# Kernel optimization log

Hardware: AMD Instinct MI355X
Metric: run time of the kernel (lower is better)

## Reference

```python
import jax, jax.numpy as jnp
import numpy as np

NUM_GRAPHS = 1024


def _mlp2(h, Wa, ba, Wb, bb):
    # Linear -> ReLU -> Linear
    return jax.nn.relu(h @ Wa + ba) @ Wb + bb


def setup_inputs() -> dict:
    key = jax.random.key(0)
    ks = jax.random.split(key, 16)
    N, F, H, C, E = 100000, 128, 128, 10, 1600000
    x = jax.random.normal(ks[0], (N, F), dtype=jnp.float32)
    edge_index = jax.random.randint(ks[1], (2, E), 0, N, dtype=jnp.int64)
    batch = jnp.sort(jax.random.randint(ks[2], (N,), 0, NUM_GRAPHS, dtype=jnp.int64))
    s = 1.0 / np.sqrt(H)
    def w(k, shape):
        return jax.random.uniform(k, shape, jnp.float32, -s, s)
    return {
        "x": x, "edge_index": edge_index, "batch": batch,
        "W1a": w(ks[3], (F, H)), "b1a": w(ks[4], (H,)),
        "W1b": w(ks[5], (H, H)), "b1b": w(ks[6], (H,)),
        "W2a": w(ks[7], (H, H)), "b2a": w(ks[8], (H,)),
        "W2b": w(ks[9], (H, H)), "b2b": w(ks[10], (H,)),
        "Wl1": w(ks[11], (H, H)), "bl1": w(ks[12], (H,)),
        "Wl2": w(ks[13], (H, C)), "bl2": w(ks[14], (C,)),
    }


def reference(x, edge_index, batch, W1a, b1a, W1b, b1b, W2a, b2a, W2b, b2b, Wl1, bl1, Wl2, bl2):
    N = x.shape[0]
    src, dst = edge_index[0], edge_index[1]

    def gin_conv(h, Wa, ba, Wb, bb):
        # sum-aggregate neighbor features: agg[i] = sum_{(src->dst=i)} h[src]
        agg = jax.ops.segment_sum(h[src], dst, num_segments=N)
        # eps = 0 (PyG default): nn((1+eps)*h + agg)
        return _mlp2(h + agg, Wa, ba, Wb, bb)

    h = jax.nn.relu(gin_conv(x, W1a, b1a, W1b, b1b))
    h = jax.nn.relu(gin_conv(h, W2a, b2a, W2b, b2b))
    # global_add_pool over graph ids -> [num_graphs, H]
    g = jax.ops.segment_sum(h, batch, num_segments=NUM_GRAPHS)
    g = jax.nn.relu(g @ Wl1 + bl1)
    return jax.nn.log_softmax(g @ Wl2 + bl2, axis=1)
```

## Files before the change

### kernel.cpp

```cpp
#include <hip/hip_runtime.h>
#include <hip/hip_bf16.h>
#include <math.h>

#define NUM_GRAPHS 1024

typedef __attribute__((ext_vector_type(8))) short bf16x8;
typedef __attribute__((ext_vector_type(4))) float f32x4;

static __device__ __forceinline__ unsigned short f2bf(float f) {
    union { float f; unsigned u; } v; v.f = f;
    unsigned r = v.u + 0x7fffu + ((v.u >> 16) & 1u);
    return (unsigned short)(r >> 16);
}
static __device__ __forceinline__ float bf_lo(unsigned u) { return __uint_as_float(u << 16); }
static __device__ __forceinline__ float bf_hi(unsigned u) { return __uint_as_float(u & 0xffff0000u); }

__global__ void k_pre(const int* __restrict__ eiDst, int E,
                      int* __restrict__ deg, int* __restrict__ rank,
                      const float* __restrict__ x, int n4, unsigned* __restrict__ xb,
                      int eb) {
    if ((int)blockIdx.x < eb) {
        int e = blockIdx.x * 256 + threadIdx.x;
        if (e < E) rank[e] = atomicAdd(&deg[eiDst[e]], 1);
    } else {
        int i = (blockIdx.x - eb) * 256 + threadIdx.x;
        int stride = (gridDim.x - eb) * 256;
        const float4* x4 = (const float4*)x;
        for (; i < n4; i += stride) {
            float4 v = x4[i];
            unsigned lo = (unsigned)f2bf(v.x) | ((unsigned)f2bf(v.y) << 16);
            unsigned hi = (unsigned)f2bf(v.z) | ((unsigned)f2bf(v.w) << 16);
            ((uint2*)xb)[i] = make_uint2(lo, hi);
        }
    }
}

__global__ void k_scan1(const int* __restrict__ deg, int N,
                        int* __restrict__ excl, int* __restrict__ bsum) {
    __shared__ int s[256];
    int i = blockIdx.x * 256 + threadIdx.x;
    int v = (i < N) ? deg[i] : 0;
    s[threadIdx.x] = v;
    __syncthreads();
    for (int off = 1; off < 256; off <<= 1) {
        int t = (threadIdx.x >= off) ? s[threadIdx.x - off] : 0;
        __syncthreads();
        s[threadIdx.x] += t;
        __syncthreads();
    }
    if (i < N) excl[i] = s[threadIdx.x] - v;
    if (threadIdx.x == 255) bsum[blockIdx.x] = s[255];
}

__global__ void k_scan2(int* __restrict__ bsum, int nb) {
    __shared__ int s[1024];
    int t = threadIdx.x;
    int v = (t < nb) ? bsum[t] : 0;
    s[t] = v;
    __syncthreads();
    for (int off = 1; off < 1024; off <<= 1) {
        int u = (t >= off) ? s[t - off] : 0;
        __syncthreads();
        s[t] += u;
        __syncthreads();
    }
    if (t < nb) bsum[t] = s[t] - v;
}

__global__ void k_scan3(const int* __restrict__ excl, const int* __restrict__ bsum,
                        int N, int E, int* __restrict__ rp) {
    int i = blockIdx.x * 256 + threadIdx.x;
    if (i < N) rp[i] = excl[i] + bsum[i >> 8];
    if (i == 0) rp[N] = E;
}

#define FILL_PASSES 3
#define FILL_RANGE 33334
__global__ void k_fill3(const int* __restrict__ ei, const int* __restrict__ rank,
                        int E, const int* __restrict__ rp, int* __restrict__ srcs) {
    const int tid0 = blockIdx.x * 256 + threadIdx.x;
    const int stride = gridDim.x * 256;
    for (int pass = 0; pass < FILL_PASSES; ++pass) {
        const int lo = pass * FILL_RANGE;
        const int hi = lo + FILL_RANGE;
        for (int e = tid0; e < E; e += stride) {
            int d = ei[(size_t)E + e];
            if (d >= lo && d < hi) {
                srcs[rp[d] + rank[e]] = ei[e];
            }
        }
    }
}

__global__ void k_prepw4(const float* __restrict__ W0, const float* __restrict__ W1,
                         const float* __restrict__ W2, const float* __restrict__ W3,
                         unsigned short* __restrict__ wt) {
    int b = blockIdx.x >> 6;
    const float* W = (b == 0) ? W0 : (b == 1) ? W1 : (b == 2) ? W2 : W3;
    int idx = (blockIdx.x & 63) * 256 + threadIdx.x;
    int k = idx >> 7, n = idx & 127;
    wt[b * 16384 + n * 128 + k] = f2bf(W[idx]);
}

__device__ __forceinline__ void acc8(float* a, uint4 v) {
    a[0] += bf_lo(v.x); a[1] += bf_hi(v.x);
    a[2] += bf_lo(v.y); a[3] += bf_hi(v.y);
    a[4] += bf_lo(v.z); a[5] += bf_hi(v.z);
    a[6] += bf_lo(v.w); a[7] += bf_hi(v.w);
}

__global__ __launch_bounds__(256, 8)
void k_aggq(const uint4* __restrict__ H4, const int* __restrict__ rp,
            const int* __restrict__ srcs, int N, uint4* __restrict__ out) {
    int gw = (blockIdx.x * blockDim.x + threadIdx.x) >> 6;
    int lane = threadIdx.x & 63;
    int q = lane >> 4, ql = lane & 15;
    int n = gw * 4 + q;
    if (gw * 4 >= N) return;
    bool act = (n < N);
    int nc = act ? n : 0;
    uint4 s0 = H4[(size_t)nc * 16 + ql];
    float a[8];
    a[0] = bf_lo(s0.x); a[1] = bf_hi(s0.x);
    a[2] = bf_lo(s0.y); a[3] = bf_hi(s0.y);
    a[4] = bf_lo(s0.z); a[5] = bf_hi(s0.z);
    a[6] = bf_lo(s0.w); a[7] = bf_hi(s0.w);
    int j = act ? rp[nc] : 0;
    int e = act ? rp[nc + 1] : 0;
    while (j + 4 <= e) {
        int i0 = srcs[j], i1 = srcs[j + 1], i2 = srcs[j + 2], i3 = srcs[j + 3];
        uint4 v0 = H4[(size_t)i0 * 16 + ql];
        uint4 v1 = H4[(size_t)i1 * 16 + ql];
        uint4 v2 = H4[(size_t)i2 * 16 + ql];
        uint4 v3 = H4[(size_t)i3 * 16 + ql];
        acc8(a, v0); acc8(a, v1); acc8(a, v2); acc8(a, v3);
        j += 4;
    }
    while (j < e) {
        uint4 v = H4[(size_t)srcs[j] * 16 + ql];
        acc8(a, v);
        ++j;
    }
    if (act) {
        uint4 o;
        o.x = (unsigned)f2bf(a[0]) | ((unsigned)f2bf(a[1]) << 16);
        o.y = (unsigned)f2bf(a[2]) | ((unsigned)f2bf(a[3]) << 16);
        o.z = (unsigned)f2bf(a[4]) | ((unsigned)f2bf(a[5]) << 16);
        o.w = (unsigned)f2bf(a[6]) | ((unsigned)f2bf(a[7]) << 16);
        out[(size_t)n * 16 + ql] = o;
    }
}

__device__ __forceinline__ int swz_base(int row, int chunk) {
    return row * 128 + ((chunk ^ (row & 7)) << 3);
}

__global__ __launch_bounds__(256, 2)
void k_mlp(const unsigned short* __restrict__ U, int N,
           const unsigned short* __restrict__ WaT, const float* __restrict__ ba,
           const unsigned short* __restrict__ WbT, const float* __restrict__ bb,
           unsigned short* __restrict__ Y) {
    __shared__ unsigned short lA[128 * 128];
    __shared__ unsigned short lW[128 * 128];

    const int tid = threadIdx.x;
    const int lane = tid & 63;
    const int w = tid >> 6;
    const int wr = (w >> 1) * 64;
    const int wc = (w & 1) * 64;
    const int r0 = blockIdx.x * 128;

    {
        const uint4* U4 = (const uint4*)U;
        #pragma unroll
        for (int i = 0; i < 8; ++i) {
            int c = tid + 256 * i;
            int row = c >> 4, q = c & 15;
            uint4 v = (r0 + row < N) ? U4[(size_t)(r0 + row) * 16 + q]
                                     : make_uint4(0u, 0u, 0u, 0u);
            *(uint4*)&lA[swz_base(row, q)] = v;
        }
    }
    {
        const uint4* Wsrc = (const uint4*)WaT;
        #pragma unroll
        for (int i = 0; i < 8; ++i) {
            int c = tid + 256 * i;
            int row = c >> 4, q = c & 15;
            *(uint4*)&lW[swz_base(row, q)] = Wsrc[c];
        }
    }
    __syncthreads();

    const int am = lane & 15;
    const int kq = (lane >> 4) * 8;

    f32x4 acc[4][4];
    #pragma unroll
    for (int i = 0; i < 4; ++i)
        #pragma unroll
        for (int j = 0; j < 4; ++j) acc[i][j] = (f32x4){0.f, 0.f, 0.f, 0.f};

    #pragma unroll
    for (int ks = 0; ks < 4; ++ks) {
        int k0 = ks * 32 + kq;
        bf16x8 af[4], bq[4];
        #pragma unroll
        for (int i = 0; i < 4; ++i)
            af[i] = *(const bf16x8*)&lA[swz_base(wr + i * 16 + am, k0 >> 3)];
        #pragma unroll
        for (int j = 0; j < 4; ++j)
            bq[j] = *(const bf16x8*)&lW[swz_base(wc + j * 16 + am, k0 >> 3)];
        #pragma unroll
        for (int i = 0; i < 4; ++i)
            #pragma unroll
            for (int j = 0; j < 4; ++j)
                acc[i][j] = __builtin_amdgcn_mfma_f32_16x16x32_bf16(af[i], bq[j], acc[i][j], 0, 0, 0);
    }
    __syncthreads();

    #pragma unroll
    for (int j = 0; j < 4; ++j) {
        int col = wc + j * 16 + am;
        float bias = ba[col];
        #pragma unroll
        for (int i = 0; i < 4; ++i) {
            int rowb = wr + i * 16 + (lane >> 4) * 4;
            #pragma unroll
            for (int r = 0; r < 4; ++r) {
                float t = acc[i][j][r] + bias;
                t = t > 0.f ? t : 0.f;
                int row = rowb + r;
                lA[swz_base(row, col >> 3) + (col & 7)] = f2bf(t);
            }
        }
    }
    {
        const uint4* Wsrc = (const uint4*)WbT;
        #pragma unroll
        for (int i = 0; i < 8; ++i) {
            int c = tid + 256 * i;
            int row = c >> 4, q = c & 15;
            *(uint4*)&lW[swz_base(row, q)] = Wsrc[c];
        }
    }
    __syncthreads();

    #pragma unroll
    for (int i = 0; i < 4; ++i)
        #pragma unroll
        for (int j = 0; j < 4; ++j) acc[i][j] = (f32x4){0.f, 0.f, 0.f, 0.f};

    #pragma unroll
    for (int ks = 0; ks < 4; ++ks) {
        int k0 = ks * 32 + kq;
        bf16x8 af[4], bq[4];
        #pragma unroll
        for (int i = 0; i < 4; ++i)
            af[i] = *(const bf16x8*)&lA[swz_base(wr + i * 16 + am, k0 >> 3)];
        #pragma unroll
        for (int j = 0; j < 4; ++j)
            bq[j] = *(const bf16x8*)&lW[swz_base(wc + j * 16 + am, k0 >> 3)];
        #pragma unroll
        for (int i = 0; i < 4; ++i)
            #pragma unroll
            for (int j = 0; j < 4; ++j)
                acc[i][j] = __builtin_amdgcn_mfma_f32_16x16x32_bf16(af[i], bq[j], acc[i][j], 0, 0, 0);
    }

    #pragma unroll
    for (int j = 0; j < 4; ++j) {
        int col = wc + j * 16 + am;
        float bias = bb[col];
        #pragma unroll
        for (int i = 0; i < 4; ++i) {
            int rowb = wr + i * 16 + (lane >> 4) * 4;
            #pragma unroll
            for (int r = 0; r < 4; ++r) {
                int row = r0 + rowb + r;
                if (row < N) {
                    float t = acc[i][j][r] + bias;
                    t = t > 0.f ? t : 0.f;
                    Y[(size_t)row * 128 + col] = f2bf(t);
                }
            }
        }
    }
}

#define PSTRIP 8
__global__ void k_pool(const unsigned* __restrict__ H, const int* __restrict__ batch,
                       int N, float* __restrict__ G) {
    int wid = (blockIdx.x * blockDim.x + threadIdx.x) >> 6;
    int lane = threadIdx.x & 63;
    int n0 = wid * PSTRIP;
    if (n0 >= N) return;
    int n1 = n0 + PSTRIP; if (n1 > N) n1 = N;
    const size_t fo = (size_t)lane * 2;
    int cur = batch[n0];
    float aL = 0.f, aH = 0.f;
    for (int n = n0; n < n1; ++n) {
        int b = batch[n];
        if (b != cur) {
            atomicAdd(&G[(size_t)cur * 128 + fo], aL);
            atomicAdd(&G[(size_t)cur * 128 + fo + 1], aH);
            aL = 0.f; aH = 0.f;
            cur = b;
        }
        unsigned v = H[(size_t)n * 64 + lane];
        aL += bf_lo(v);
        aH += bf_hi(v);
    }
    atomicAdd(&G[(size_t)cur * 128 + fo], aL);
    atomicAdd(&G[(size_t)cur * 128 + fo + 1], aH);
}

__global__ void k_head(const float* __restrict__ G,
                       const float* __restrict__ Wl1, const float* __restrict__ bl1,
                       const float* __restrict__ Wl2, const float* __restrict__ bl2,
                       int C, float* __restrict__ out) {
    __shared__ float sg[128];
    __shared__ float sh[128];
    __shared__ float sl[16];
    int row = blockIdx.x;
    int t = threadIdx.x;
    sg[t] = G[(size_t)row * 128 + t];
    __syncthreads();
    float a = bl1[t];
    for (int k = 0; k < 128; ++k) a += sg[k] * Wl1[k * 128 + t];
    sh[t] = a > 0.f ? a : 0.f;
    __syncthreads();
    if (t < C) {
        float l = bl2[t];
        for (int k = 0; k < 128; ++k) l += sh[k] * Wl2[k * C + t];
        sl[t] = l;
    }
    __syncthreads();
    if (t < C) {
        float m = -1e30f;
        for (int j = 0; j < C; ++j) m = fmaxf(m, sl[j]);
        float s = 0.f;
        for (int j = 0; j < C; ++j) s += __expf(sl[j] - m);
        out[(size_t)row * C + t] = sl[t] - m - __logf(s);
    }
}

extern "C" void kernel_launch(void* const* d_in, const int* in_sizes, int n_in,
                              void* d_out, int out_size, void* d_ws, size_t ws_size,
                              hipStream_t stream) {
    const float* x    = (const float*)d_in[0];
    const int*   ei   = (const int*)d_in[1];
    const int*   batch= (const int*)d_in[2];
    const float* W1a  = (const float*)d_in[3];
    const float* b1a  = (const float*)d_in[4];
    const float* W1b  = (const float*)d_in[5];
    const float* b1b  = (const float*)d_in[6];
    const float* W2a  = (const float*)d_in[7];
    const float* b2a  = (const float*)d_in[8];
    const float* W2b  = (const float*)d_in[9];
    const float* b2b  = (const float*)d_in[10];
    const float* Wl1  = (const float*)d_in[11];
    const float* bl1  = (const float*)d_in[12];
    const float* Wl2  = (const float*)d_in[13];
    const float* bl2  = (const float*)d_in[14];
    float* out = (float*)d_out;

    const int N = in_sizes[2];
    const int E = in_sizes[1] / 2;
    const int C = in_sizes[13] / 128;

    char* p = (char*)d_ws;
    auto alloc = [&](size_t bytes) {
        char* r = p;
        p += (bytes + 255) & ~(size_t)255;
        return r;
    };
    unsigned* xb = (unsigned*)alloc((size_t)N * 64 * 4);
    unsigned* hA = (unsigned*)alloc((size_t)N * 64 * 4);
    unsigned* hB = (unsigned*)alloc((size_t)N * 64 * 4);
    float* g   = (float*)alloc((size_t)NUM_GRAPHS * 128 * 4);
    int* deg   = (int*)alloc((size_t)N * 4);
    int* excl  = (int*)alloc((size_t)N * 4);
    int* rp    = (int*)alloc((size_t)(N + 1) * 4);
    int* rank  = (int*)alloc((size_t)E * 4);
    int* bsum  = (int*)alloc(4096);
    int* srcs  = (int*)alloc((size_t)E * 4);
    unsigned short* wt = (unsigned short*)alloc((size_t)4 * 16384 * 2);
    (void)ws_size; (void)n_in; (void)out_size;

    const int nb = (N + 255) / 256;
    const int eb = (E + 255) / 256;

    hipMemsetAsync(deg, 0, (size_t)N * 4, stream);
    hipMemsetAsync(g, 0, (size_t)NUM_GRAPHS * 128 * 4, stream);

    k_pre<<<eb + 4096, 256, 0, stream>>>(ei + E, E, deg, rank, x, N * 32, xb, eb);
    k_scan1<<<nb, 256, 0, stream>>>(deg, N, excl, bsum);
    k_scan2<<<1, 1024, 0, stream>>>(bsum, nb);
    k_scan3<<<nb, 256, 0, stream>>>(excl, bsum, N, E, rp);
    k_fill3<<<2048, 256, 0, stream>>>(ei, rank, E, rp, srcs);
    k_prepw4<<<256, 256, 0, stream>>>(W1a, W1b, W2a, W2b, wt);

    const int mb = (N + 127) / 128;
    const int qw = (N + 3) / 4;
    const int qb = (qw + 3) / 4;

    k_aggq<<<qb, 256, 0, stream>>>((const uint4*)xb, rp, srcs, N, (uint4*)hA);
    k_mlp<<<mb, 256, 0, stream>>>((const unsigned short*)hA, N, wt, b1a, wt + 16384, b1b,
                                  (unsigned short*)hB);
    k_aggq<<<qb, 256, 0, stream>>>((const uint4*)hB, rp, srcs, N, (uint4*)hA);
    k_mlp<<<mb, 256, 0, stream>>>((const unsigned short*)hA, N, wt + 2 * 16384, b2a,
                                  wt + 3 * 16384, b2b, (unsigned short*)hB);

    const int pw = (N + PSTRIP - 1) / PSTRIP;
    const int pb = (pw + 3) / 4;
    k_pool<<<pb, 256, 0, stream>>>(hB, batch, N, g);
    k_head<<<NUM_GRAPHS, 128, 0, stream>>>(g, Wl1, bl1, Wl2, bl2, C, out);
}
```

Baseline: 439.1 us.

## Fuse global pooling into second MLP and merge small setup kernels

```diff
diff --git a/kernel.cpp b/kernel.cpp
--- a/kernel.cpp
+++ b/kernel.cpp
@@ -18,13 +18,13 @@
 __global__ void k_pre(const int* __restrict__ eiDst, int E,
                       int* __restrict__ deg, int* __restrict__ rank,
                       const float* __restrict__ x, int n4, unsigned* __restrict__ xb,
-                      int eb) {
+                      float* __restrict__ G, int eb) {
     if ((int)blockIdx.x < eb) {
         int e = blockIdx.x * 256 + threadIdx.x;
         if (e < E) rank[e] = atomicAdd(&deg[eiDst[e]], 1);
-    } else {
+    } else if ((int)blockIdx.x < eb + 4096) {
         int i = (blockIdx.x - eb) * 256 + threadIdx.x;
-        int stride = (gridDim.x - eb) * 256;
+        int stride = 4096 * 256;
         const float4* x4 = (const float4*)x;
         for (; i < n4; i += stride) {
             float4 v = x4[i];
@@ -32,6 +32,11 @@
             unsigned hi = (unsigned)f2bf(v.z) | ((unsigned)f2bf(v.w) << 16);
             ((uint2*)xb)[i] = make_uint2(lo, hi);
         }
+    } else {
+        int i = (blockIdx.x - eb - 4096) * 256 + threadIdx.x;
+        float4* G4 = (float4*)G;
+        for (; i < NUM_GRAPHS * 32; i += 64 * 256)
+            G4[i] = make_float4(0.f, 0.f, 0.f, 0.f);
     }
 }
 
@@ -52,54 +57,58 @@
     if (threadIdx.x == 255) bsum[blockIdx.x] = s[255];
 }
 
-__global__ void k_scan2(int* __restrict__ bsum, int nb) {
-    __shared__ int s[1024];
-    int t = threadIdx.x;
-    int v = (t < nb) ? bsum[t] : 0;
-    s[t] = v;
-    __syncthreads();
-    for (int off = 1; off < 1024; off <<= 1) {
-        int u = (t >= off) ? s[t - off] : 0;
-        __syncthreads();
-        s[t] += u;
-        __syncthreads();
-    }
-    if (t < nb) bsum[t] = s[t] - v;
-}
-
-__global__ void k_scan3(const int* __restrict__ excl, const int* __restrict__ bsum,
-                        int N, int E, int* __restrict__ rp) {
-    int i = blockIdx.x * 256 + threadIdx.x;
-    if (i < N) rp[i] = excl[i] + bsum[i >> 8];
+__global__ void k_scan23(const int* __restrict__ excl, const int* __restrict__ bsum,
+                         int nb, int N, int E, int* __restrict__ rp) {
+    __shared__ int s[512];
+    const int t = threadIdx.x;
+    for (int k = t; k < 512; k += 256) s[k] = (k < nb) ? bsum[k] : 0;
+    __syncthreads();
+    #pragma unroll
+    for (int off = 1; off < 512; off <<= 1) {
+        int a = (t >= off) ? s[t - off] : 0;
+        int b = s[t + 256 - off];
+        __syncthreads();
+        s[t] += a;
+        s[t + 256] += b;
+        __syncthreads();
+    }
+    const int myIncl = s[blockIdx.x];
+    const int myOwn = bsum[blockIdx.x];
+    const int off_b = myIncl - myOwn;
+    int i = blockIdx.x * 256 + t;
+    if (i < N) rp[i] = excl[i] + off_b;
     if (i == 0) rp[N] = E;
 }
 
 #define FILL_PASSES 3
 #define FILL_RANGE 33334
-__global__ void k_fill3(const int* __restrict__ ei, const int* __restrict__ rank,
-                        int E, const int* __restrict__ rp, int* __restrict__ srcs) {
-    const int tid0 = blockIdx.x * 256 + threadIdx.x;
-    const int stride = gridDim.x * 256;
-    for (int pass = 0; pass < FILL_PASSES; ++pass) {
-        const int lo = pass * FILL_RANGE;
-        const int hi = lo + FILL_RANGE;
-        for (int e = tid0; e < E; e += stride) {
-            int d = ei[(size_t)E + e];
-            if (d >= lo && d < hi) {
-                srcs[rp[d] + rank[e]] = ei[e];
+#define FILL_BLOCKS 2048
+__global__ void k_fillprep(const int* __restrict__ ei, const int* __restrict__ rank,
+                           int E, const int* __restrict__ rp, int* __restrict__ srcs,
+                           const float* __restrict__ W0, const float* __restrict__ W1,
+                           const float* __restrict__ W2, const float* __restrict__ W3,
+                           unsigned short* __restrict__ wt) {
+    if ((int)blockIdx.x < FILL_BLOCKS) {
+        const int tid0 = blockIdx.x * 256 + threadIdx.x;
+        const int stride = FILL_BLOCKS * 256;
+        for (int pass = 0; pass < FILL_PASSES; ++pass) {
+            const int lo = pass * FILL_RANGE;
+            const int hi = lo + FILL_RANGE;
+            for (int e = tid0; e < E; e += stride) {
+                int d = ei[(size_t)E + e];
+                if (d >= lo && d < hi) {
+                    srcs[rp[d] + rank[e]] = ei[e];
+                }
             }
         }
-    }
-}
-
-__global__ void k_prepw4(const float* __restrict__ W0, const float* __restrict__ W1,
-                         const float* __restrict__ W2, const float* __restrict__ W3,
-                         unsigned short* __restrict__ wt) {
-    int b = blockIdx.x >> 6;
-    const float* W = (b == 0) ? W0 : (b == 1) ? W1 : (b == 2) ? W2 : W3;
-    int idx = (blockIdx.x & 63) * 256 + threadIdx.x;
-    int k = idx >> 7, n = idx & 127;
-    wt[b * 16384 + n * 128 + k] = f2bf(W[idx]);
+    } else {
+        int lb = blockIdx.x - FILL_BLOCKS;
+        int b = lb >> 6;
+        const float* W = (b == 0) ? W0 : (b == 1) ? W1 : (b == 2) ? W2 : W3;
+        int idx = (lb & 63) * 256 + threadIdx.x;
+        int k = idx >> 7, n = idx & 127;
+        wt[b * 16384 + n * 128 + k] = f2bf(W[idx]);
+    }
 }
 
 __device__ __forceinline__ void acc8(float* a, uint4 v) {
@@ -155,13 +164,16 @@
     return row * 128 + ((chunk ^ (row & 7)) << 3);
 }
 
+template <bool POOL>
 __global__ __launch_bounds__(256, 2)
 void k_mlp(const unsigned short* __restrict__ U, int N,
            const unsigned short* __restrict__ WaT, const float* __restrict__ ba,
            const unsigned short* __restrict__ WbT, const float* __restrict__ bb,
-           unsigned short* __restrict__ Y) {
+           unsigned short* __restrict__ Y,
+           const int* __restrict__ batch, float* __restrict__ G) {
     __shared__ unsigned short lA[128 * 128];
     __shared__ unsigned short lW[128 * 128];
+    __shared__ int bs[128];
 
     const int tid = threadIdx.x;
     const int lane = tid & 63;
@@ -268,51 +280,62 @@
                 acc[i][j] = __builtin_amdgcn_mfma_f32_16x16x32_bf16(af[i], bq[j], acc[i][j], 0, 0, 0);
     }
 
-    #pragma unroll
-    for (int j = 0; j < 4; ++j) {
-        int col = wc + j * 16 + am;
-        float bias = bb[col];
-        #pragma unroll
-        for (int i = 0; i < 4; ++i) {
-            int rowb = wr + i * 16 + (lane >> 4) * 4;
+    if (!POOL) {
+        #pragma unroll
+        for (int j = 0; j < 4; ++j) {
+            int col = wc + j * 16 + am;
+            float bias = bb[col];
             #pragma unroll
-            for (int r = 0; r < 4; ++r) {
-                int row = r0 + rowb + r;
-                if (row < N) {
+            for (int i = 0; i < 4; ++i) {
+                int rowb = wr + i * 16 + (lane >> 4) * 4;
+                #pragma unroll
+                for (int r = 0; r < 4; ++r) {
+                    int row = r0 + rowb + r;
+                    if (row < N) {
+                        float t = acc[i][j][r] + bias;
+                        t = t > 0.f ? t : 0.f;
+                        Y[(size_t)row * 128 + col] = f2bf(t);
+                    }
+                }
+            }
+        }
+    } else {
+        __syncthreads();
+        #pragma unroll
+        for (int j = 0; j < 4; ++j) {
+            int col = wc + j * 16 + am;
+            float bias = bb[col];
+            #pragma unroll
+            for (int i = 0; i < 4; ++i) {
+                int rowb = wr + i * 16 + (lane >> 4) * 4;
+                #pragma unroll
+                for (int r = 0; r < 4; ++r) {
                     float t = acc[i][j][r] + bias;
                     t = t > 0.f ? t : 0.f;
-                    Y[(size_t)row * 128 + col] = f2bf(t);
+                    int row = rowb + r;
+                    lA[swz_base(row, col >> 3) + (col & 7)] = f2bf(t);
                 }
             }
         }
-    }
-}
-
-#define PSTRIP 8
-__global__ void k_pool(const unsigned* __restrict__ H, const int* __restrict__ batch,
-                       int N, float* __restrict__ G) {
-    int wid = (blockIdx.x * blockDim.x + threadIdx.x) >> 6;
-    int lane = threadIdx.x & 63;
-    int n0 = wid * PSTRIP;
-    if (n0 >= N) return;
-    int n1 = n0 + PSTRIP; if (n1 > N) n1 = N;
-    const size_t fo = (size_t)lane * 2;
-    int cur = batch[n0];
-    float aL = 0.f, aH = 0.f;
-    for (int n = n0; n < n1; ++n) {
-        int b = batch[n];
-        if (b != cur) {
-            atomicAdd(&G[(size_t)cur * 128 + fo], aL);
-            atomicAdd(&G[(size_t)cur * 128 + fo + 1], aH);
-            aL = 0.f; aH = 0.f;
-            cur = b;
-        }
-        unsigned v = H[(size_t)n * 64 + lane];
-        aL += bf_lo(v);
-        aH += bf_hi(v);
-    }
-    atomicAdd(&G[(size_t)cur * 128 + fo], aL);
-    atomicAdd(&G[(size_t)cur * 128 + fo + 1], aH);
+        if (tid < 128) bs[tid] = (r0 + tid < N) ? batch[r0 + tid] : -1;
+        __syncthreads();
+        const int col = tid & 127;
+        const int half = tid >> 7;
+        const int rbeg = half * 64, rend = rbeg + 64;
+        float pacc = 0.f;
+        int cur = bs[rbeg];
+        for (int row = rbeg; row < rend; ++row) {
+            int b = bs[row];
+            if (b != cur) {
+                if (cur >= 0) atomicAdd(&G[(size_t)cur * 128 + col], pacc);
+                pacc = 0.f;
+                cur = b;
+            }
+            unsigned short u = lA[swz_base(row, col >> 3) + (col & 7)];
+            pacc += __uint_as_float((unsigned)u << 16);
+        }
+        if (cur >= 0) atomicAdd(&G[(size_t)cur * 128 + col], pacc);
+    }
 }
 
 __global__ void k_head(const float* __restrict__ G,
@@ -392,28 +415,24 @@
     const int eb = (E + 255) / 256;
 
     hipMemsetAsync(deg, 0, (size_t)N * 4, stream);
-    hipMemsetAsync(g, 0, (size_t)NUM_GRAPHS * 128 * 4, stream);
-
-    k_pre<<<eb + 4096, 256, 0, stream>>>(ei + E, E, deg, rank, x, N * 32, xb, eb);
+
+    k_pre<<<eb + 4096 + 64, 256, 0, stream>>>(ei + E, E, deg, rank, x, N * 32, xb, g, eb);
     k_scan1<<<nb, 256, 0, stream>>>(deg, N, excl, bsum);
-    k_scan2<<<1, 1024, 0, stream>>>(bsum, nb);
-    k_scan3<<<nb, 256, 0, stream>>>(excl, bsum, N, E, rp);
-    k_fill3<<<2048, 256, 0, stream>>>(ei, rank, E, rp, srcs);
-    k_prepw4<<<256, 256, 0, stream>>>(W1a, W1b, W2a, W2b, wt);
+    k_scan23<<<nb, 256, 0, stream>>>(excl, bsum, nb, N, E, rp);
+    k_fillprep<<<FILL_BLOCKS + 256, 256, 0, stream>>>(ei, rank, E, rp, srcs,
+                                                      W1a, W1b, W2a, W2b, wt);
 
     const int mb = (N + 127) / 128;
     const int qw = (N + 3) / 4;
     const int qb = (qw + 3) / 4;
 
     k_aggq<<<qb, 256, 0, stream>>>((const uint4*)xb, rp, srcs, N, (uint4*)hA);
-    k_mlp<<<mb, 256, 0, stream>>>((const unsigned short*)hA, N, wt, b1a, wt + 16384, b1b,
-                                  (unsigned short*)hB);
+    k_mlp<false><<<mb, 256, 0, stream>>>((const unsigned short*)hA, N, wt, b1a,
+                                         wt + 16384, b1b, (unsigned short*)hB,
+                                         nullptr, nullptr);
     k_aggq<<<qb, 256, 0, stream>>>((const uint4*)hB, rp, srcs, N, (uint4*)hA);
-    k_mlp<<<mb, 256, 0, stream>>>((const unsigned short*)hA, N, wt + 2 * 16384, b2a,
-                                  wt + 3 * 16384, b2b, (unsigned short*)hB);
-
-    const int pw = (N + PSTRIP - 1) / PSTRIP;
-    const int pb = (pw + 3) / 4;
-    k_pool<<<pb, 256, 0, stream>>>(hB, batch, N, g);
+    k_mlp<true><<<mb, 256, 0, stream>>>((const unsigned short*)hA, N, wt + 2 * 16384, b2a,
+                                        wt + 3 * 16384, b2b, nullptr,
+                                        batch, g);
     k_head<<<NUM_GRAPHS, 128, 0, stream>>>(g, Wl1, bl1, Wl2, bl2, C, out);
 }
```

Measured after the change: 419.8 us. -4.4%, faster.
